# Kernel tuning notes

Hardware: AMD Instinct MI355X
Metric: run time of the kernel (lower is better)

Reference implementation:

```python
import jax, jax.numpy as jnp
import numpy as np

N = 50000      # nodes
E = 1000000    # edges
NF = 5         # node_features
EF = 2         # edge_features
RS = 128       # rnn_size
RES = 32       # rnn_edge_size
H = 4          # heads
C = 16         # out_features
FIN = RS + RES # GAT in_channels
NEG_SLOPE = 0.2


def lstm_step(x, h, c, Wih, Whh, bih, bhh):
    # Single-step LSTM (torch gate order: i, f, g, o)
    g = x @ Wih.T + h @ Whh.T + bih + bhh
    i, f, gg, o = jnp.split(g, 4, axis=-1)
    i = jax.nn.sigmoid(i); f = jax.nn.sigmoid(f)
    gg = jnp.tanh(gg); o = jax.nn.sigmoid(o)
    c2 = f * c + i * gg
    return o * jnp.tanh(c2), c2


def setup_inputs() -> dict:
    key = jax.random.key(0)
    ks = jax.random.split(key, 20)
    p = lambda k, shape: (jax.random.normal(k, shape) * 0.1).astype(jnp.float32)
    return dict(
        x=jax.random.normal(ks[0], (N, NF), jnp.float32),
        edge_index=jax.random.randint(ks[1], (2, E), 0, N),
        edge_attr=jax.random.normal(ks[2], (E, EF), jnp.float32),
        h_node_h=p(ks[3], (N, RS)), h_node_c=p(ks[4], (N, RS)),
        h_edge_h=p(ks[5], (E, RES)), h_edge_c=p(ks[6], (E, RES)),
        Wih_n=p(ks[7], (4 * RS, NF)), Whh_n=p(ks[8], (4 * RS, RS)),
        bih_n=p(ks[9], (4 * RS,)), bhh_n=p(ks[10], (4 * RS,)),
        Wih_e=p(ks[11], (4 * RES, EF)), Whh_e=p(ks[12], (4 * RES, RES)),
        bih_e=p(ks[13], (4 * RES,)), bhh_e=p(ks[14], (4 * RES,)),
        W_gat=p(ks[15], (FIN, H * C)),
        att_src=p(ks[16], (H, C)), att_dst=p(ks[17], (H, C)),
        bias_gat=p(ks[18], (C,)),
    )


def reference(x, edge_index, edge_attr, h_node_h, h_node_c, h_edge_h, h_edge_c,
              Wih_n, Whh_n, bih_n, bhh_n, Wih_e, Whh_e, bih_e, bhh_e,
              W_gat, att_src, att_dst, bias_gat):
    n = x.shape[0]
    # --- edge history encoder: per-edge LSTM step + scatter-mean to dst nodes ---
    he, ce = lstm_step(edge_attr, h_edge_h, h_edge_c, Wih_e, Whh_e, bih_e, bhh_e)
    dst0 = edge_index[1]
    esum = jax.ops.segment_sum(he, dst0, num_segments=n)
    deg = jax.ops.segment_sum(jnp.ones((he.shape[0], 1), he.dtype), dst0, num_segments=n)
    edge_enc = esum / jnp.maximum(deg, 1.0)            # [N, RES]
    # --- node history encoder: per-node LSTM step ---
    hn, cn = lstm_step(x, h_node_h, h_node_c, Wih_n, Whh_n, bih_n, bhh_n)
    feat = jnp.concatenate([hn, edge_enc], axis=-1)    # [N, FIN]
    # --- GATConv (PyG v1 style, add_self_loops=True, concat=False) ---
    xl = (feat @ W_gat).reshape(n, H, C)               # [N, H, C]
    a_src = jnp.einsum('nhc,hc->nh', xl, att_src)
    a_dst = jnp.einsum('nhc,hc->nh', xl, att_dst)
    loops = jnp.arange(n)
    src = jnp.concatenate([edge_index[0], loops])
    dst = jnp.concatenate([edge_index[1], loops])
    alpha = jax.nn.leaky_relu(a_src[src] + a_dst[dst], NEG_SLOPE)  # [E+N, H]
    m = jax.ops.segment_max(alpha, dst, num_segments=n)
    ea = jnp.exp(alpha - m[dst])
    s = jax.ops.segment_sum(ea, dst, num_segments=n)
    w = ea / s[dst]                                     # segment softmax over dst
    out = jax.ops.segment_sum(xl[src] * w[:, :, None], dst, num_segments=n)  # [N,H,C]
    out = out.mean(axis=1) + bias_gat                   # concat=False -> head mean
    return (out, hn, cn, he, ce)
```

## Files before the change

kernel.cpp:

```cpp
#include <hip/hip_runtime.h>

#define CAP 64

typedef __attribute__((ext_vector_type(8))) short bf16x8;
typedef __attribute__((ext_vector_type(4))) float f32x4;

__device__ __forceinline__ float sigf(float x) {
    return __builtin_amdgcn_rcpf(1.0f + __expf(-x));
}
__device__ __forceinline__ float tanhfast(float x) {
    return 2.0f * __builtin_amdgcn_rcpf(1.0f + __expf(-2.0f * x)) - 1.0f;
}
__device__ __forceinline__ short bfr(float f) {
    unsigned u = __float_as_uint(f);
    unsigned r = (u + 0x7FFFu + ((u >> 16) & 1u)) >> 16;
    return (short)r;
}
__device__ __forceinline__ float bf2f(unsigned short u) {
    return __uint_as_float(((unsigned)u) << 16);
}
__device__ __forceinline__ bf16x8 cvt8(const float* p) {
    const float4* q = (const float4*)p;
    float4 u = q[0], v = q[1];
    bf16x8 r;
    r[0]=bfr(u.x); r[1]=bfr(u.y); r[2]=bfr(u.z); r[3]=bfr(u.w);
    r[4]=bfr(v.x); r[5]=bfr(v.y); r[6]=bfr(v.z); r[7]=bfr(v.w);
    return r;
}

__global__ void convert_kernel(
    const float* __restrict__ Whh_n, const float* __restrict__ Wih_n,
    const float* __restrict__ bih_n, const float* __restrict__ bhh_n,
    const float* __restrict__ Whh_e, const float* __restrict__ Wih_e,
    const float* __restrict__ bih_e, const float* __restrict__ bhh_e,
    const float* __restrict__ Wgat,
    unsigned short* __restrict__ WnF, unsigned short* __restrict__ WeF,
    unsigned short* __restrict__ WgF, int* __restrict__ cnt, int N)
{
    int i = blockIdx.x * 256 + threadIdx.x;
    if (i < N) cnt[i] = 0;
    if (i < 512 * 160) {
        int j = i & 7, unit = i >> 3;
        int lane = unit & 63, tk = unit >> 6;
        int tp = tk / 5, k4 = tk - tp * 5;
        int r = (tp & 3) * 128 + (tp >> 2) * 16 + (lane & 15);
        int k = k4 * 32 + (lane >> 4) * 8 + j;
        float v = (k < 128) ? Whh_n[r * 128 + k]
                : (k < 133) ? Wih_n[r * 5 + (k - 128)]
                : (k == 133) ? (bih_n[r] + bhh_n[r]) : 0.f;
        WnF[i] = (unsigned short)bfr(v);
    }
    if (i < 128 * 64) {
        int j = i & 7, unit = i >> 3;
        int lane = unit & 63, ts = unit >> 6;
        int t = ts >> 1, s = ts & 1;
        int r = t * 16 + (lane & 15);
        int k = s * 32 + (lane >> 4) * 8 + j;
        float v = (k < 32) ? Whh_e[r * 32 + k]
                : (k < 34) ? Wih_e[r * 2 + (k - 32)]
                : (k == 34) ? (bih_e[r] + bhh_e[r]) : 0.f;
        WeF[i] = (unsigned short)bfr(v);
    }
    if (i < 64 * 160) {
        int j = i & 7, unit = i >> 3;
        int lane = unit & 63, tk = unit >> 6;
        int t = tk / 5, k4 = tk - t * 5;
        int r = t * 16 + (lane & 15);
        int k = k4 * 32 + (lane >> 4) * 8 + j;
        WgF[i] = (unsigned short)bfr(Wgat[k * 64 + r]);
    }
}

__global__ void csr_fill_kernel(const int* __restrict__ src, const int* __restrict__ dst,
                                int* __restrict__ cnt, int2* __restrict__ eidp, int E)
{
    int e = blockIdx.x * blockDim.x + threadIdx.x;
    if (e >= E) return;
    int d = dst[e];
    int s = src[e];
    int k = atomicAdd(cnt + d, 1);
    if (k < CAP) eidp[(size_t)d * CAP + k] = make_int2(e, s);
}

__global__ __launch_bounds__(256, 3) void edge_lstm_mfma(
    const float* __restrict__ eattr, const float* __restrict__ h_in, const float* __restrict__ c_in,
    const unsigned short* __restrict__ WeF,
    float* __restrict__ he_out, float* __restrict__ ce_out, int E)
{
    __shared__ float Gall[4][16 * 132];
    __shared__ unsigned short Hall[4][16 * 40];
    const int lane = threadIdx.x & 63, wave = threadIdx.x >> 6;
    const int lr = lane & 15, lg = lane >> 4;
    const int T = E >> 4;
    const int nwaves = gridDim.x * 4;
    const int wid = blockIdx.x * 4 + wave;
    if (wid >= T) return;
    float* G = Gall[wave];
    unsigned short* H = Hall[wave];

    const bf16x8* Wv = (const bf16x8*)WeF;
    bf16x8 wa0[8], wa1[8];
    #pragma unroll
    for (int t = 0; t < 8; ++t) {
        wa0[t] = Wv[(t * 2 + 0) * 64 + lane];
        wa1[t] = Wv[(t * 2 + 1) * 64 + lane];
    }

    f32x4 phA, phB, pcA, pcB; float pea0 = 0.f, pea1 = 0.f;
    {
        const size_t dwb = (size_t)wid * 512;
        phA = *(const f32x4*)(h_in + dwb + lane * 4);
        phB = *(const f32x4*)(h_in + dwb + 256 + lane * 4);
        pcA = *(const f32x4*)(c_in + dwb + lane * 4);
        pcB = *(const f32x4*)(c_in + dwb + 256 + lane * 4);
        if (lg == 0) {
            pea0 = eattr[(size_t)(wid * 16 + lr) * 2];
            pea1 = eattr[(size_t)(wid * 16 + lr) * 2 + 1];
        }
    }

    for (int t = wid; t < T; t += nwaves) {
        const f32x4 hA = phA, hB = phB, cA = pcA, cB = pcB;
        const float ea0 = pea0, ea1 = pea1;
        const size_t dwbase = (size_t)t * 512;
        const int tn = t + nwaves;
        if (tn < T) {
            const size_t dwb = (size_t)tn * 512;
            phA = *(const f32x4*)(h_in + dwb + lane * 4);
            phB = *(const f32x4*)(h_in + dwb + 256 + lane * 4);
            pcA = *(const f32x4*)(c_in + dwb + lane * 4);
            pcB = *(const f32x4*)(c_in + dwb + 256 + lane * 4);
            if (lg == 0) {
                pea0 = eattr[(size_t)(tn * 16 + lr) * 2];
                pea1 = eattr[(size_t)(tn * 16 + lr) * 2 + 1];
            }
        }

        {
            const int e = lane >> 3, c4 = (lane & 7) * 4;
            ushort4 pa, pb;
            pa.x = (unsigned short)bfr(hA[0]); pa.y = (unsigned short)bfr(hA[1]);
            pa.z = (unsigned short)bfr(hA[2]); pa.w = (unsigned short)bfr(hA[3]);
            pb.x = (unsigned short)bfr(hB[0]); pb.y = (unsigned short)bfr(hB[1]);
            pb.z = (unsigned short)bfr(hB[2]); pb.w = (unsigned short)bfr(hB[3]);
            *(ushort4*)(H + e * 40 + c4)       = pa;
            *(ushort4*)(H + (8 + e) * 40 + c4) = pb;
        }
        bf16x8 b0 = *(const bf16x8*)(H + lr * 40 + lg * 8);
        bf16x8 b1 = {0,0,0,0,0,0,0,0};
        if (lg == 0) {
            b1[0] = bfr(ea0); b1[1] = bfr(ea1); b1[2] = (short)0x3F80;
        }

        f32x4 acc[8];
        #pragma unroll
        for (int tt = 0; tt < 8; ++tt) {
            f32x4 v = {0, 0, 0, 0};
            v = __builtin_amdgcn_mfma_f32_16x16x32_bf16(wa0[tt], b0, v, 0, 0, 0);
            v = __builtin_amdgcn_mfma_f32_16x16x32_bf16(wa1[tt], b1, v, 0, 0, 0);
            acc[tt] = v;
        }

        #pragma unroll
        for (int u = 0; u < 8; ++u) {
            const int col = (u >> 1) * 32 + (u & 1) * 16 + lg * 4;
            *(f32x4*)(G + lr * 132 + col) = acc[u];
        }

        const int e = lane >> 3, jq = (lane & 7) * 4;
        #pragma unroll
        for (int part = 0; part < 2; ++part) {
            const float* gr = G + (part * 8 + e) * 132;
            const f32x4 gi = *(const f32x4*)(gr + jq);
            const f32x4 gf = *(const f32x4*)(gr + 32 + jq);
            const f32x4 gg = *(const f32x4*)(gr + 64 + jq);
            const f32x4 go = *(const f32x4*)(gr + 96 + jq);
            const f32x4 cold = part ? cB : cA;
            f32x4 cres, hres;
            #pragma unroll
            for (int q = 0; q < 4; ++q) {
                float c2 = sigf(gf[q]) * cold[q] + sigf(gi[q]) * tanhfast(gg[q]);
                cres[q] = c2;
                hres[q] = sigf(go[q]) * tanhfast(c2);
            }
            __builtin_nontemporal_store(cres, (f32x4*)(ce_out + dwbase + part * 256 + lane * 4));
            *(f32x4*)(he_out + dwbase + part * 256 + lane * 4) = hres;
        }
    }
}

__global__ __launch_bounds__(256) void node_lstm_mfma(
    const float* __restrict__ x, const float* __restrict__ h_in, const float* __restrict__ c_in,
    const unsigned short* __restrict__ WnF,
    float* __restrict__ hn_out, float* __restrict__ cn_out, int N)
{
    const int lane = threadIdx.x & 63, wave = threadIdx.x >> 6;
    const int nbase = blockIdx.x * 64 + wave * 16;
    if (nbase >= N) return;
    const int lr = lane & 15, lg = lane >> 4;
    const int node = nbase + lr;
    bf16x8 b[5];
    const float* hp = h_in + (size_t)node * 128 + lg * 8;
    b[0] = cvt8(hp); b[1] = cvt8(hp + 32); b[2] = cvt8(hp + 64); b[3] = cvt8(hp + 96);
    bf16x8 bx = {0,0,0,0,0,0,0,0};
    if (lg == 0) {
        const float* xp = x + (size_t)node * 5;
        bx[0]=bfr(xp[0]); bx[1]=bfr(xp[1]); bx[2]=bfr(xp[2]); bx[3]=bfr(xp[3]); bx[4]=bfr(xp[4]);
        bx[5] = (short)0x3F80;
    }
    b[4] = bx;
    const bf16x8* Wv = (const bf16x8*)WnF;
    #pragma unroll
    for (int u = 0; u < 8; ++u) {
        f32x4 acc[4];
        #pragma unroll
        for (int g = 0; g < 4; ++g) {
            const bf16x8* ap = Wv + (u * 4 + g) * 320 + lane;
            f32x4 v = {0, 0, 0, 0};
            #pragma unroll
            for (int k4 = 0; k4 < 5; ++k4)
                v = __builtin_amdgcn_mfma_f32_16x16x32_bf16(ap[k4 * 64], b[k4], v, 0, 0, 0);
            acc[g] = v;
        }
        const int jb = u * 16 + lg * 4;
        f32x4 cold = *(const f32x4*)(c_in + (size_t)node * 128 + jb);
        f32x4 cres, hres;
        #pragma unroll
        for (int q = 0; q < 4; ++q) {
            float c2 = sigf(acc[1][q]) * cold[q] + sigf(acc[0][q]) * tanhfast(acc[2][q]);
            cres[q] = c2;
            hres[q] = sigf(acc[3][q]) * tanhfast(c2);
        }
        __builtin_nontemporal_store(cres, (f32x4*)(cn_out + (size_t)node * 128 + jb));
        *(f32x4*)(hn_out + (size_t)node * 128 + jb) = hres;
    }
}

__global__ __launch_bounds__(256) void enc_gatxl_kernel(
    const int* __restrict__ cnt, const int2* __restrict__ eidp, const float* __restrict__ he,
    const float* __restrict__ hn, const unsigned short* __restrict__ WgF,
    const float* __restrict__ attS, const float* __restrict__ attD,
    unsigned short* __restrict__ xlb, float* __restrict__ asrc, float* __restrict__ adst, int N)
{
    __shared__ float encs[64 * 36];
    const int lane = threadIdx.x & 63, wave = threadIdx.x >> 6;
    const int nbase = blockIdx.x * 64 + wave * 16;
    if (nbase >= N) return;
    const int half = lane >> 5, hl = lane & 31;
    const int g4 = hl >> 3, l8 = hl & 7;
    for (int t = 0; t < 16; t += 2) {
        const int node = nbase + t + half;
        const int c = cnt[node];
        const int m = min(c, CAP);
        const int2* el = eidp + (size_t)node * CAP;
        f32x4 acc = {0, 0, 0, 0};
        for (int i = g4; i < m; i += 4)
            acc += *(const f32x4*)(he + (size_t)el[i].x * 32 + l8 * 4);
        #pragma unroll
        for (int off = 8; off <= 16; off <<= 1) {
            acc[0] += __shfl_xor(acc[0], off);
            acc[1] += __shfl_xor(acc[1], off);
            acc[2] += __shfl_xor(acc[2], off);
            acc[3] += __shfl_xor(acc[3], off);
        }
        if (g4 == 0) {
            float inv = 1.0f / fmaxf((float)c, 1.0f);
            f32x4 r; r[0]=acc[0]*inv; r[1]=acc[1]*inv; r[2]=acc[2]*inv; r[3]=acc[3]*inv;
            *(f32x4*)(&encs[(wave * 16 + t + half) * 36 + l8 * 4]) = r;
        }
    }
    const int lr = lane & 15, lg = lane >> 4;
    const int node = nbase + lr;
    bf16x8 b[5];
    const float* hp = hn + (size_t)node * 128 + lg * 8;
    b[0] = cvt8(hp); b[1] = cvt8(hp + 32); b[2] = cvt8(hp + 64); b[3] = cvt8(hp + 96);
    b[4] = cvt8(&encs[(wave * 16 + lr) * 36 + lg * 8]);
    const bf16x8* Wv = (const bf16x8*)WgF;
    #pragma unroll
    for (int t = 0; t < 4; ++t) {
        const bf16x8* ap = Wv + t * 320 + lane;
        f32x4 v = {0, 0, 0, 0};
        #pragma unroll
        for (int k4 = 0; k4 < 5; ++k4)
            v = __builtin_amdgcn_mfma_f32_16x16x32_bf16(ap[k4 * 64], b[k4], v, 0, 0, 0);
        ushort4 pk;
        pk.x = (unsigned short)bfr(v[0]); pk.y = (unsigned short)bfr(v[1]);
        pk.z = (unsigned short)bfr(v[2]); pk.w = (unsigned short)bfr(v[3]);
        *(ushort4*)(xlb + (size_t)node * 64 + t * 16 + lg * 4) = pk;
        const f32x4 ws = *(const f32x4*)(attS + t * 16 + lg * 4);
        const f32x4 wd = *(const f32x4*)(attD + t * 16 + lg * 4);
        float p1 = v[0]*ws[0] + v[1]*ws[1] + v[2]*ws[2] + v[3]*ws[3];
        float p2 = v[0]*wd[0] + v[1]*wd[1] + v[2]*wd[2] + v[3]*wd[3];
        p1 += __shfl_xor(p1, 16); p2 += __shfl_xor(p2, 16);
        p1 += __shfl_xor(p1, 32); p2 += __shfl_xor(p2, 32);
        if (lg == 0) {
            asrc[(size_t)node * 4 + t] = p1;
            adst[(size_t)node * 4 + t] = p2;
        }
    }
}

__global__ __launch_bounds__(256) void gat_node_kernel(
    const int* __restrict__ cnt, const int2* __restrict__ eidp,
    const float* __restrict__ asrc, const float* __restrict__ adst,
    const unsigned short* __restrict__ xlb, const float* __restrict__ bias,
    float* __restrict__ out, int N)
{
    const int wid = (blockIdx.x * blockDim.x + threadIdx.x) >> 6;
    const int lane = threadIdx.x & 63;
    if (wid >= N) return;
    const int n = wid;
    const int m = min(cnt[n], CAP);
    const int h = lane >> 4, c16 = lane & 15;
    const int nslot = (m + 15) >> 4;
    const float ad = adst[n * 4 + h];
    float aself = asrc[n * 4 + h] + ad;
    aself = aself > 0.f ? aself : 0.2f * aself;
    const int2* el = eidp + (size_t)n * CAP;
    int   ss[4];
    float aa[4];
    float mx = aself;
    #pragma unroll
    for (int k = 0; k < 4; ++k) {
        if (k >= nslot) break;
        int i = k * 16 + c16;
        if (i < m) {
            int s = el[i].y;
            float a = asrc[s * 4 + h] + ad;
            a = a > 0.f ? a : 0.2f * a;
            ss[k] = s; aa[k] = a;
            mx = fmaxf(mx, a);
        } else { ss[k] = 0; aa[k] = -1e30f; }
    }
    #pragma unroll
    for (int off = 1; off < 16; off <<= 1) mx = fmaxf(mx, __shfl_xor(mx, off));
    float ea[4];
    float p = 0.f;
    #pragma unroll
    for (int k = 0; k < 4; ++k) {
        if (k >= nslot) break;
        ea[k] = __expf(aa[k] - mx);
        p += ea[k];
    }
    #pragma unroll
    for (int off = 1; off < 16; off <<= 1) p += __shfl_xor(p, off);
    float eself = __expf(aself - mx);
    float sacc = eself + p;
    float oacc = eself * bf2f(xlb[(size_t)n * 64 + lane]);
    const int grp = lane & 48;
    #pragma unroll
    for (int k = 0; k < 4; ++k) {
        if (k >= nslot) break;
        const int lim = min(16, m - k * 16);
        #pragma unroll 4
        for (int cc = 0; cc < lim; ++cc) {
            int srcl = grp | cc;
            float w = __shfl(ea[k], srcl);
            int   s = __shfl(ss[k], srcl);
            oacc += w * bf2f(xlb[(size_t)s * 64 + lane]);
        }
    }
    float r = oacc / sacc;
    r += __shfl_xor(r, 16);
    r += __shfl_xor(r, 32);
    if (lane < 16) out[(size_t)n * 16 + lane] = 0.25f * r + bias[lane];
}

extern "C" void kernel_launch(void* const* d_in, const int* in_sizes, int n_in,
                              void* d_out, int out_size, void* d_ws, size_t ws_size,
                              hipStream_t stream)
{
    const float* x     = (const float*)d_in[0];
    const int*   ei    = (const int*)  d_in[1];
    const float* eattr = (const float*)d_in[2];
    const float* hn_h  = (const float*)d_in[3];
    const float* hn_c  = (const float*)d_in[4];
    const float* he_h  = (const float*)d_in[5];
    const float* he_c  = (const float*)d_in[6];
    const float* Wih_n = (const float*)d_in[7];
    const float* Whh_n = (const float*)d_in[8];
    const float* bih_n = (const float*)d_in[9];
    const float* bhh_n = (const float*)d_in[10];
    const float* Wih_e = (const float*)d_in[11];
    const float* Whh_e = (const float*)d_in[12];
    const float* bih_e = (const float*)d_in[13];
    const float* bhh_e = (const float*)d_in[14];
    const float* W_gat = (const float*)d_in[15];
    const float* attS  = (const float*)d_in[16];
    const float* attD  = (const float*)d_in[17];
    const float* biasG = (const float*)d_in[18];

    const int N = in_sizes[0] / 5;
    const int E = in_sizes[2] / 2;

    float* out = (float*)d_out;
    float* hn  = out + (size_t)N * 16;
    float* cn  = hn  + (size_t)N * 128;
    float* he  = cn  + (size_t)N * 128;
    float* ce  = he  + (size_t)E * 32;

    char* p = (char*)d_ws;
    size_t off = 0;
    auto take = [&](size_t bytes) -> void* {
        void* r = p + off;
        off = (off + bytes + 255) & ~(size_t)255;
        return r;
    };
    int*   cnt  = (int*)  take((size_t)N * 4);
    int2*  eidp = (int2*) take((size_t)N * CAP * 8);
    unsigned short* xlb = (unsigned short*)take((size_t)N * 64 * 2);
    float* asrc = (float*)take((size_t)N * 4 * 4);
    float* adst = (float*)take((size_t)N * 4 * 4);
    unsigned short* WnF = (unsigned short*)take(512 * 160 * 2);
    unsigned short* WeF = (unsigned short*)take(128 * 64 * 2);
    unsigned short* WgF = (unsigned short*)take(64 * 160 * 2);

    convert_kernel<<<(512 * 160 + 255) / 256, 256, 0, stream>>>(
        Whh_n, Wih_n, bih_n, bhh_n, Whh_e, Wih_e, bih_e, bhh_e, W_gat,
        WnF, WeF, WgF, cnt, N);
    csr_fill_kernel<<<(E + 255) / 256, 256, 0, stream>>>(ei, ei + E, cnt, eidp, E);
    edge_lstm_mfma<<<768, 256, 0, stream>>>(
        eattr, he_h, he_c, WeF, he, ce, E);
    node_lstm_mfma<<<(N + 63) / 64, 256, 0, stream>>>(
        x, hn_h, hn_c, WnF, hn, cn, N);
    enc_gatxl_kernel<<<(N + 63) / 64, 256, 0, stream>>>(
        cnt, eidp, he, hn, WgF, attS, attD, xlb, asrc, adst, N);
    gat_node_kernel<<<(N + 3) / 4, 256, 0, stream>>>(
        cnt, eidp, asrc, adst, xlb, biasG, out, N);
}
```

Measured before the change: 351.1 us.

## Fuse weight conversion with CSR fill, widen scatter-mean gather, unroll aggregation

Merges the weight-conversion and CSR-fill kernels into one launch and moves the count reset to a memset, removing one kernel launch boundary. The edge-encoder mean now has all 64 lanes gather one node's edges at once, each lane loading 8 floats, with a full-wave shuffle reduction instead of half-wave groups. The GAT neighbour aggregation loop unroll goes from 4 to 8. In exchange the reduction needs more shuffle steps per node and the unrolled loop uses more registers.

```diff
diff --git a/kernel.cpp b/kernel.cpp
--- a/kernel.cpp
+++ b/kernel.cpp
@@ -28,58 +28,59 @@
     return r;
 }
 
-__global__ void convert_kernel(
+__global__ void setup_kernel(
     const float* __restrict__ Whh_n, const float* __restrict__ Wih_n,
     const float* __restrict__ bih_n, const float* __restrict__ bhh_n,
     const float* __restrict__ Whh_e, const float* __restrict__ Wih_e,
     const float* __restrict__ bih_e, const float* __restrict__ bhh_e,
     const float* __restrict__ Wgat,
     unsigned short* __restrict__ WnF, unsigned short* __restrict__ WeF,
-    unsigned short* __restrict__ WgF, int* __restrict__ cnt, int N)
-{
-    int i = blockIdx.x * 256 + threadIdx.x;
-    if (i < N) cnt[i] = 0;
-    if (i < 512 * 160) {
-        int j = i & 7, unit = i >> 3;
-        int lane = unit & 63, tk = unit >> 6;
-        int tp = tk / 5, k4 = tk - tp * 5;
-        int r = (tp & 3) * 128 + (tp >> 2) * 16 + (lane & 15);
-        int k = k4 * 32 + (lane >> 4) * 8 + j;
-        float v = (k < 128) ? Whh_n[r * 128 + k]
-                : (k < 133) ? Wih_n[r * 5 + (k - 128)]
-                : (k == 133) ? (bih_n[r] + bhh_n[r]) : 0.f;
-        WnF[i] = (unsigned short)bfr(v);
-    }
-    if (i < 128 * 64) {
-        int j = i & 7, unit = i >> 3;
-        int lane = unit & 63, ts = unit >> 6;
-        int t = ts >> 1, s = ts & 1;
-        int r = t * 16 + (lane & 15);
-        int k = s * 32 + (lane >> 4) * 8 + j;
-        float v = (k < 32) ? Whh_e[r * 32 + k]
-                : (k < 34) ? Wih_e[r * 2 + (k - 32)]
-                : (k == 34) ? (bih_e[r] + bhh_e[r]) : 0.f;
-        WeF[i] = (unsigned short)bfr(v);
-    }
-    if (i < 64 * 160) {
-        int j = i & 7, unit = i >> 3;
-        int lane = unit & 63, tk = unit >> 6;
-        int t = tk / 5, k4 = tk - t * 5;
-        int r = t * 16 + (lane & 15);
-        int k = k4 * 32 + (lane >> 4) * 8 + j;
-        WgF[i] = (unsigned short)bfr(Wgat[k * 64 + r]);
-    }
-}
-
-__global__ void csr_fill_kernel(const int* __restrict__ src, const int* __restrict__ dst,
-                                int* __restrict__ cnt, int2* __restrict__ eidp, int E)
-{
-    int e = blockIdx.x * blockDim.x + threadIdx.x;
-    if (e >= E) return;
-    int d = dst[e];
-    int s = src[e];
-    int k = atomicAdd(cnt + d, 1);
-    if (k < CAP) eidp[(size_t)d * CAP + k] = make_int2(e, s);
+    unsigned short* __restrict__ WgF,
+    const int* __restrict__ src, const int* __restrict__ dst,
+    int* __restrict__ cnt, int2* __restrict__ eidp, int E)
+{
+    const int B = blockIdx.x;
+    if (B < 320) {
+        int i = B * 256 + threadIdx.x;
+        if (i < 512 * 160) {
+            int j = i & 7, unit = i >> 3;
+            int lane = unit & 63, tk = unit >> 6;
+            int tp = tk / 5, k4 = tk - tp * 5;
+            int r = (tp & 3) * 128 + (tp >> 2) * 16 + (lane & 15);
+            int k = k4 * 32 + (lane >> 4) * 8 + j;
+            float v = (k < 128) ? Whh_n[r * 128 + k]
+                    : (k < 133) ? Wih_n[r * 5 + (k - 128)]
+                    : (k == 133) ? (bih_n[r] + bhh_n[r]) : 0.f;
+            WnF[i] = (unsigned short)bfr(v);
+        }
+        if (i < 128 * 64) {
+            int j = i & 7, unit = i >> 3;
+            int lane = unit & 63, ts = unit >> 6;
+            int t = ts >> 1, s = ts & 1;
+            int r = t * 16 + (lane & 15);
+            int k = s * 32 + (lane >> 4) * 8 + j;
+            float v = (k < 32) ? Whh_e[r * 32 + k]
+                    : (k < 34) ? Wih_e[r * 2 + (k - 32)]
+                    : (k == 34) ? (bih_e[r] + bhh_e[r]) : 0.f;
+            WeF[i] = (unsigned short)bfr(v);
+        }
+        if (i < 64 * 160) {
+            int j = i & 7, unit = i >> 3;
+            int lane = unit & 63, tk = unit >> 6;
+            int t = tk / 5, k4 = tk - t * 5;
+            int r = t * 16 + (lane & 15);
+            int k = k4 * 32 + (lane >> 4) * 8 + j;
+            WgF[i] = (unsigned short)bfr(Wgat[k * 64 + r]);
+        }
+    } else {
+        int e = (B - 320) * 256 + threadIdx.x;
+        if (e < E) {
+            int d = dst[e];
+            int s = src[e];
+            int k = atomicAdd(cnt + d, 1);
+            if (k < CAP) eidp[(size_t)d * CAP + k] = make_int2(e, s);
+        }
+    }
 }
 
 __global__ __launch_bounds__(256, 3) void edge_lstm_mfma(
@@ -246,27 +247,39 @@
     const int lane = threadIdx.x & 63, wave = threadIdx.x >> 6;
     const int nbase = blockIdx.x * 64 + wave * 16;
     if (nbase >= N) return;
-    const int half = lane >> 5, hl = lane & 31;
-    const int g4 = hl >> 3, l8 = hl & 7;
-    for (int t = 0; t < 16; t += 2) {
-        const int node = nbase + t + half;
+    const int rg = lane >> 2;
+    const int q8 = (lane & 3) * 8;
+    #pragma unroll 2
+    for (int t = 0; t < 16; ++t) {
+        const int node = nbase + t;
         const int c = cnt[node];
         const int m = min(c, CAP);
         const int2* el = eidp + (size_t)node * CAP;
-        f32x4 acc = {0, 0, 0, 0};
-        for (int i = g4; i < m; i += 4)
-            acc += *(const f32x4*)(he + (size_t)el[i].x * 32 + l8 * 4);
-        #pragma unroll
-        for (int off = 8; off <= 16; off <<= 1) {
-            acc[0] += __shfl_xor(acc[0], off);
-            acc[1] += __shfl_xor(acc[1], off);
-            acc[2] += __shfl_xor(acc[2], off);
-            acc[3] += __shfl_xor(acc[3], off);
-        }
-        if (g4 == 0) {
+        f32x4 a0 = {0, 0, 0, 0}, a1 = {0, 0, 0, 0};
+        #pragma unroll
+        for (int s = 0; s < 4; ++s) {
+            const int i = s * 16 + rg;
+            if (i < m) {
+                const float* hr = he + (size_t)el[i].x * 32 + q8;
+                a0 += *(const f32x4*)(hr);
+                a1 += *(const f32x4*)(hr + 4);
+            }
+        }
+        #pragma unroll
+        for (int off = 4; off < 64; off <<= 1) {
+            a0[0] += __shfl_xor(a0[0], off); a0[1] += __shfl_xor(a0[1], off);
+            a0[2] += __shfl_xor(a0[2], off); a0[3] += __shfl_xor(a0[3], off);
+            a1[0] += __shfl_xor(a1[0], off); a1[1] += __shfl_xor(a1[1], off);
+            a1[2] += __shfl_xor(a1[2], off); a1[3] += __shfl_xor(a1[3], off);
+        }
+        if (lane < 4) {
             float inv = 1.0f / fmaxf((float)c, 1.0f);
-            f32x4 r; r[0]=acc[0]*inv; r[1]=acc[1]*inv; r[2]=acc[2]*inv; r[3]=acc[3]*inv;
-            *(f32x4*)(&encs[(wave * 16 + t + half) * 36 + l8 * 4]) = r;
+            f32x4 r0, r1;
+            #pragma unroll
+            for (int q = 0; q < 4; ++q) { r0[q] = a0[q] * inv; r1[q] = a1[q] * inv; }
+            float* er = &encs[(wave * 16 + t) * 36 + q8];
+            *(f32x4*)(er)     = r0;
+            *(f32x4*)(er + 4) = r1;
         }
     }
     const int lr = lane & 15, lg = lane >> 4;
@@ -352,7 +365,7 @@
     for (int k = 0; k < 4; ++k) {
         if (k >= nslot) break;
         const int lim = min(16, m - k * 16);
-        #pragma unroll 4
+        #pragma unroll 8
         for (int cc = 0; cc < lim; ++cc) {
             int srcl = grp | cc;
             float w = __shfl(ea[k], srcl);
@@ -415,10 +428,10 @@
     unsigned short* WeF = (unsigned short*)take(128 * 64 * 2);
     unsigned short* WgF = (unsigned short*)take(64 * 160 * 2);
 
-    convert_kernel<<<(512 * 160 + 255) / 256, 256, 0, stream>>>(
+    hipMemsetAsync(cnt, 0, (size_t)N * 4, stream);
+    setup_kernel<<<320 + (E + 255) / 256, 256, 0, stream>>>(
         Whh_n, Wih_n, bih_n, bhh_n, Whh_e, Wih_e, bih_e, bhh_e, W_gat,
-        WnF, WeF, WgF, cnt, N);
-    csr_fill_kernel<<<(E + 255) / 256, 256, 0, stream>>>(ei, ei + E, cnt, eidp, E);
+        WnF, WeF, WgF, ei, ei + E, cnt, eidp, E);
     edge_lstm_mfma<<<768, 256, 0, stream>>>(
         eattr, he_h, he_c, WeF, he, ce, E);
     node_lstm_mfma<<<(N + 63) / 64, 256, 0, stream>>>(
```

Measured after the change: 358.2 us. 2.0% more time.
